# Performance work log

Measured on AMD Instinct MI355X. Metric: run time of the kernel, lower is better.

Reference implementation:

```python
import jax, jax.numpy as jnp
import numpy as np

N = 100000
NEG_SLOPE = 0.2
EPS = 1e-16


def _gatconv(h_in, src, dst, W, a_src, a_dst, b):
    # h_in: [N, Fin]; src/dst: [E_tot] (self-loops included); W: [Fin, Fout]
    h = h_in @ W                                  # [N, Fout]
    alpha_s = h @ a_src                           # [N]
    alpha_d = h @ a_dst                           # [N]
    e = alpha_s[src] + alpha_d[dst]               # [E_tot]
    e = jnp.where(e > 0, e, NEG_SLOPE * e)        # leaky_relu
    m = jax.ops.segment_max(e, dst, num_segments=N)
    e = jnp.exp(e - m[dst])
    s = jax.ops.segment_sum(e, dst, num_segments=N)
    alpha = e / (s[dst] + EPS)                    # segment softmax over in-edges of each dst
    out = jax.ops.segment_sum(alpha[:, None] * h[src], dst, num_segments=N)
    return out + b


def setup_inputs() -> dict:
    key = jax.random.key(0)
    ks = jax.random.split(key, 10)
    Fin, Fh, Fo = 64, 64, 40
    E = 1600000
    x = jax.random.normal(ks[0], (N, Fin), dtype=jnp.float32)
    edge_index = jax.random.randint(ks[1], (2, E), 0, N, dtype=jnp.int64)
    g = 1.0 / np.sqrt(Fin)
    W1 = jax.random.uniform(ks[2], (Fin, Fh), jnp.float32, -g, g)
    a_src1 = jax.random.uniform(ks[3], (Fh,), jnp.float32, -g, g)
    a_dst1 = jax.random.uniform(ks[4], (Fh,), jnp.float32, -g, g)
    b1 = jnp.zeros((Fh,), jnp.float32)
    g2 = 1.0 / np.sqrt(Fh)
    W2 = jax.random.uniform(ks[5], (Fh, Fo), jnp.float32, -g2, g2)
    a_src2 = jax.random.uniform(ks[6], (Fo,), jnp.float32, -g2, g2)
    a_dst2 = jax.random.uniform(ks[7], (Fo,), jnp.float32, -g2, g2)
    b2 = jnp.zeros((Fo,), jnp.float32)
    return {"x": x, "edge_index": edge_index, "W1": W1, "a_src1": a_src1,
            "a_dst1": a_dst1, "b1": b1, "W2": W2, "a_src2": a_src2,
            "a_dst2": a_dst2, "b2": b2}


def reference(x, edge_index, W1, a_src1, a_dst1, b1, W2, a_src2, a_dst2, b2):
    # add self loops (PyG GATConv default)
    loops = jnp.arange(N, dtype=edge_index.dtype)
    src = jnp.concatenate([edge_index[0], loops])
    dst = jnp.concatenate([edge_index[1], loops])
    h = _gatconv(x, src, dst, W1, a_src1, a_dst1, b1)
    h = jax.nn.relu(h)  # dropout p=0 / eval -> no-op
    h = _gatconv(h, src, dst, W2, a_src2, a_dst2, b2)
    return jax.nn.log_softmax(h, axis=-1)
```

## Files before the change

kernel.cpp:

```cpp
#include <hip/hip_runtime.h>
#include <math.h>

#ifndef NEG_SLOPE
#define NEG_SLOPE 0.2f
#endif

#define BUCK_BITS 9
#define BUCK_SIZE 512
#define BUCK_CAP  12288
#define PA_ILP    8
#define SMAX      0x1FFFF

typedef __attribute__((ext_vector_type(8))) short bhalf8;
typedef __attribute__((ext_vector_type(4))) float f32x4;

__device__ __forceinline__ void get_edge(const void* ei, int is64, int e, int E,
                                         int& s, int& d) {
    if (e >= E) { s = e - E; d = s; return; }
    if (is64) {
        const long long* p = (const long long*)ei;
        s = (int)p[e];
        d = (int)p[(long long)E + e];
    } else {
        const int* p = (const int*)ei;
        s = p[e];
        d = p[E + e];
    }
}

__device__ __forceinline__ unsigned f2bf1(float x) {
    unsigned u = __float_as_uint(x);
    return (u + 0x7fffu + ((u >> 16) & 1u)) >> 16;
}

__global__ __launch_bounds__(256) void bin_gemm1(
    const void* __restrict__ ei, int E, int Etot, int binB, int gemmB, int period,
    int* __restrict__ fill, unsigned* __restrict__ pairs,
    const float* __restrict__ x, const float* __restrict__ W1,
    const float* __restrict__ avs, const float* __restrict__ avd,
    unsigned short* __restrict__ Hb, float* __restrict__ asn,
    float* __restrict__ adn, int N) {
    __shared__ __align__(16) char smem[16896];
    const int t = threadIdx.x;
    const int bi = blockIdx.x;
    const bool isBin = (bi % period) == 0;

    if (isBin) {
        const int bb = bi / period;
        int* cnt   = (int*)smem;
        int* goff  = cnt + 256;
        int* sflag = goff + 256;
        if (t < 64) {
            const int* p = (const int*)ei;
            int bad = 0;
            for (int j = 0; j < 4; ++j) bad |= (p[2 * (t * 4 + j) + 1] != 0);
            unsigned long long m = __ballot(bad);
            if (t == 0) *sflag = (m == 0ull) ? 1 : 0;
        }
        cnt[t] = 0;
        __syncthreads();
        const int is64 = *sflag;
        const int base = bb * (256 * PA_ILP) + t;
        int s[PA_ILP], d[PA_ILP], r[PA_ILP];
        bool ok[PA_ILP];
#pragma unroll
        for (int u = 0; u < PA_ILP; ++u) {
            int e = base + u * 256;
            ok[u] = (e < Etot);
            s[u] = d[u] = 0;
            if (ok[u]) get_edge(ei, is64, e, E, s[u], d[u]);
        }
#pragma unroll
        for (int u = 0; u < PA_ILP; ++u)
            if (ok[u]) r[u] = atomicAdd(&cnt[d[u] >> BUCK_BITS], 1);
        __syncthreads();
        if (cnt[t] > 0) goff[t] = atomicAdd(&fill[t], cnt[t]);
        __syncthreads();
#pragma unroll
        for (int u = 0; u < PA_ILP; ++u) {
            if (ok[u]) {
                int b = d[u] >> BUCK_BITS;
                int idx = goff[b] + r[u];
                if (idx < BUCK_CAP)
                    pairs[(size_t)b * BUCK_CAP + idx] =
                        (unsigned)s[u] | ((unsigned)(d[u] & (BUCK_SIZE - 1)) << 17);
            }
        }
    } else {
        const int gi = bi - bi / period - 1;
        if (gi >= gemmB) return;
        constexpr int K = 64, F = 64, TPR = 4, R = 64, C = 16;
        float* sW  = (float*)smem;
        float* sas = sW + K * F;
        float* sad = sas + F;

        for (int i = t; i < K * F / 4; i += 256)
            ((float4*)sW)[i] = ((const float4*)W1)[i];
        if (t < F) { sas[t] = avs[t]; sad[t] = avd[t]; }
        __syncthreads();

        const int base = gi * R;
        const int r  = t / TPR;
        const int f0 = (t % TPR) * C;
        const int row = base + r;
        float acc[C];
#pragma unroll
        for (int j = 0; j < C; ++j) acc[j] = 0.f;
        if (row < N) {
            const float4* xr = (const float4*)(x + (size_t)row * K);
#pragma unroll
            for (int c4 = 0; c4 < 16; ++c4) {
                float4 a = xr[c4];
                const float* w0 = &sW[(c4 * 4 + 0) * F + f0];
                const float* w1 = &sW[(c4 * 4 + 1) * F + f0];
                const float* w2 = &sW[(c4 * 4 + 2) * F + f0];
                const float* w3 = &sW[(c4 * 4 + 3) * F + f0];
#pragma unroll
                for (int j = 0; j < C; ++j)
                    acc[j] += a.x * w0[j] + a.y * w1[j] + a.z * w2[j] + a.w * w3[j];
            }
        }
        float ps = 0.f, pd = 0.f;
#pragma unroll
        for (int j = 0; j < C; ++j) { ps += acc[j] * sas[f0 + j]; pd += acc[j] * sad[f0 + j]; }
#pragma unroll
        for (int off = 1; off < TPR; off <<= 1) {
            ps += __shfl_xor(ps, off);
            pd += __shfl_xor(pd, off);
        }
        if (row < N) {
            if ((t % TPR) == 0) { asn[row] = ps; adn[row] = pd; }
            unsigned* hp = (unsigned*)(Hb + (size_t)row * F + f0);
#pragma unroll
            for (int j = 0; j < C / 2; ++j)
                hp[j] = f2bf1(acc[2 * j]) | (f2bf1(acc[2 * j + 1]) << 16);
        }
    }
}

__global__ __launch_bounds__(256) void bucket_csr(
    const unsigned* __restrict__ pairs, const int* __restrict__ fill,
    int* __restrict__ row_ptr, int* __restrict__ csr_src, int N, int nbuck) {
    __shared__ int cnt[BUCK_SIZE];
    __shared__ int offs[BUCK_SIZE];
    __shared__ int sbase[256];
    __shared__ int stot;
    const int t = threadIdx.x;
    if (t < 64) {
        int v[4];
        int loc = 0;
#pragma unroll
        for (int i = 0; i < 4; ++i) {
            int idx = t * 4 + i;
            v[i] = (idx < nbuck) ? fill[idx] : 0;
            loc += v[i];
        }
        int x = loc;
        for (int off = 1; off < 64; off <<= 1) {
            int y = __shfl_up(x, off);
            if (t >= off) x += y;
        }
        int run = x - loc;
#pragma unroll
        for (int i = 0; i < 4; ++i) {
            int idx = t * 4 + i;
            if (idx < 256) sbase[idx] = run;
            run += v[i];
        }
        if (t == 63) stot = x;
    }
    cnt[t] = 0; cnt[t + 256] = 0;
    __syncthreads();

    const int b = blockIdx.x;
    const int gb = sbase[b];
    int m = fill[b];
    if (m > BUCK_CAP) m = BUCK_CAP;
    if (b == 0 && t == 0) row_ptr[N] = stot;
    const unsigned* bp = pairs + (size_t)b * BUCK_CAP;

    int i = t;
    for (; i + 768 < m; i += 1024) {
        unsigned p0 = bp[i], p1 = bp[i + 256], p2 = bp[i + 512], p3 = bp[i + 768];
        atomicAdd(&cnt[p0 >> 17], 1);
        atomicAdd(&cnt[p1 >> 17], 1);
        atomicAdd(&cnt[p2 >> 17], 1);
        atomicAdd(&cnt[p3 >> 17], 1);
    }
    for (; i < m; i += 256) atomicAdd(&cnt[bp[i] >> 17], 1);
    __syncthreads();

    if (t < 64) {
        int v[8];
        int loc = 0;
#pragma unroll
        for (int j = 0; j < 8; ++j) { v[j] = cnt[t * 8 + j]; loc += v[j]; }
        int x = loc;
        for (int off = 1; off < 64; off <<= 1) {
            int y = __shfl_up(x, off);
            if (t >= off) x += y;
        }
        int run = x - loc;
#pragma unroll
        for (int j = 0; j < 8; ++j) { offs[t * 8 + j] = gb + run; run += v[j]; }
    }
    __syncthreads();

    const int base_d = b << BUCK_BITS;
    for (int k = t; k < BUCK_SIZE; k += 256) {
        int d = base_d + k;
        if (d < N) row_ptr[d] = offs[k];
    }
    __syncthreads();

    i = t;
    for (; i + 768 < m; i += 1024) {
        unsigned p0 = bp[i], p1 = bp[i + 256], p2 = bp[i + 512], p3 = bp[i + 768];
        csr_src[atomicAdd(&offs[p0 >> 17], 1)] = p0 & SMAX;
        csr_src[atomicAdd(&offs[p1 >> 17], 1)] = p1 & SMAX;
        csr_src[atomicAdd(&offs[p2 >> 17], 1)] = p2 & SMAX;
        csr_src[atomicAdd(&offs[p3 >> 17], 1)] = p3 & SMAX;
    }
    for (; i < m; i += 256) {
        unsigned p = bp[i];
        csr_src[atomicAdd(&offs[p >> 17], 1)] = p & SMAX;
    }
}

__device__ __forceinline__ void bf16x8_fma(uint4 hv, float w, float* acc) {
    const unsigned* u = (const unsigned*)&hv;
#pragma unroll
    for (int i = 0; i < 4; ++i) {
        float lo = __uint_as_float(u[i] << 16);
        float hi = __uint_as_float(u[i] & 0xffff0000u);
        acc[2 * i]     += w * lo;
        acc[2 * i + 1] += w * hi;
    }
}

__global__ __launch_bounds__(256) void agg1_gemm2(
    const int* __restrict__ row_ptr, const int* __restrict__ csr_src,
    const float* __restrict__ asn1, const float* __restrict__ adn1,
    const unsigned short* __restrict__ Hb, const float* __restrict__ b1,
    const float* __restrict__ W2, const float* __restrict__ a_s2,
    const float* __restrict__ a_d2, unsigned short* __restrict__ Hb2,
    float* __restrict__ asn2, float* __restrict__ adn2, int N) {
    __shared__ __align__(16) unsigned short rb16[16][72];
    __shared__ float sa2[48], sd2[48], sb1[64];
    __shared__ float sps3[3][16], spd3[3][16];
    const int t = threadIdx.x;
    if (t < 48) {
        sa2[t] = (t < 40) ? a_s2[t] : 0.f;
        sd2[t] = (t < 40) ? a_d2[t] : 0.f;
    }
    if (t >= 64 && t < 128) sb1[t - 64] = b1[t - 64];

    const int lane = t & 63;
    const int wv   = t >> 6;
    const int tile = (wv < 3) ? wv : 0;

    bhalf8 bfr[2];
    {
        const int col = tile * 16 + (lane & 15);
        const int kb  = (lane >> 4) * 8;
        const bool cv = col < 40;
#pragma unroll
        for (int ks = 0; ks < 2; ++ks) {
            bhalf8 bb;
#pragma unroll
            for (int j = 0; j < 8; ++j) {
                float v = cv ? W2[(size_t)(kb + 32 * ks + j) * 40 + col] : 0.f;
                bb[j] = (short)f2bf1(v);
            }
            bfr[ks] = bb;
        }
    }
    __syncthreads();

    const int sub     = lane & 15;
    const int half    = sub >> 3;
    const int q       = sub & 7;
    const int grpbase = lane & 48;
    const int slot    = t >> 4;
    const int node    = blockIdx.x * 16 + slot;
    const bool valid  = node < N;
    const int nd      = valid ? node : N - 1;

    const int r0 = row_ptr[nd], r1 = row_ptr[nd + 1];
    const int deg = r1 - r0;
    const float add = adn1[nd];

    float acc[8];
#pragma unroll
    for (int i = 0; i < 8; ++i) acc[i] = 0.f;

    int   sA = 0, sB = 0;
    float wA = 0.f, wB = 0.f;
    {
        const bool vA = sub < deg;
        const bool vB = 16 + sub < deg;
        if (vA) sA = csr_src[r0 + sub];
        if (vB) sB = csr_src[r0 + 16 + sub];
        float aA = vA ? asn1[sA] : 0.f;
        float aB = vB ? asn1[sB] : 0.f;
        if (vA) { float v = aA + add; v = v > 0.f ? v : NEG_SLOPE * v; wA = __expf(v); }
        if (vB) { float v = aB + add; v = v > 0.f ? v : NEG_SLOPE * v; wB = __expf(v); }
    }
    float Ssum = wA + wB;

    {
        const int cnt = deg < 16 ? deg : 16;
        int se[8]; float we[8]; uint4 hv[8];
#pragma unroll
        for (int k = 0; k < 8; ++k) {
            int e = 2 * k + half;
            int sl = grpbase | (e & 15);
            se[k] = __shfl(sA, sl);
            float wk = __shfl(wA, sl);
            we[k] = (e < cnt) ? wk : 0.f;
        }
#pragma unroll
        for (int k = 0; k < 4; ++k)
            hv[k] = *(const uint4*)(Hb + (((unsigned)se[k] << 6) | (unsigned)(q << 3)));
        if (cnt > 8) {
#pragma unroll
            for (int k = 4; k < 8; ++k)
                hv[k] = *(const uint4*)(Hb + (((unsigned)se[k] << 6) | (unsigned)(q << 3)));
        }
#pragma unroll
        for (int k = 0; k < 4; ++k) bf16x8_fma(hv[k], we[k], acc);
        if (cnt > 8) {
#pragma unroll
            for (int k = 4; k < 8; ++k) bf16x8_fma(hv[k], we[k], acc);
        }
    }
    if (deg > 16) {
        const int cnt = (deg - 16) < 16 ? (deg - 16) : 16;
        int se[8]; float we[8]; uint4 hv[8];
#pragma unroll
        for (int k = 0; k < 8; ++k) {
            int e = 2 * k + half;
            int sl = grpbase | (e & 15);
            se[k] = __shfl(sB, sl);
            float wk = __shfl(wB, sl);
            we[k] = (e < cnt) ? wk : 0.f;
        }
#pragma unroll
        for (int k = 0; k < 4; ++k)
            hv[k] = *(const uint4*)(Hb + (((unsigned)se[k] << 6) | (unsigned)(q << 3)));
        if (cnt > 8) {
#pragma unroll
            for (int k = 4; k < 8; ++k)
                hv[k] = *(const uint4*)(Hb + (((unsigned)se[k] << 6) | (unsigned)(q << 3)));
        }
#pragma unroll
        for (int k = 0; k < 4; ++k) bf16x8_fma(hv[k], we[k], acc);
        if (cnt > 8) {
#pragma unroll
            for (int k = 4; k < 8; ++k) bf16x8_fma(hv[k], we[k], acc);
        }
    }
    for (int base = r0 + 32; base < r1; base += 16) {
        int cnt = r1 - base;
        if (cnt > 16) cnt = 16;
        int s = 0;
        float w = 0.f;
        if (sub < cnt) {
            s = csr_src[base + sub];
            float v = asn1[s] + add;
            v = v > 0.f ? v : NEG_SLOPE * v;
            w = __expf(v);
        }
        Ssum += w;
        for (int j = 0; j < cnt; j += 8) {
            int se[4]; float we[4]; uint4 hv[4];
#pragma unroll
            for (int k = 0; k < 4; ++k) {
                int e = j + 2 * k + half;
                int src_lane = grpbase | (e & 15);
                se[k] = __shfl(s, src_lane);
                float wk = __shfl(w, src_lane);
                we[k] = (e < cnt) ? wk : 0.f;
            }
#pragma unroll
            for (int k = 0; k < 4; ++k)
                hv[k] = *(const uint4*)(Hb + (((unsigned)se[k] << 6) | (unsigned)(q << 3)));
#pragma unroll
            for (int k = 0; k < 4; ++k) bf16x8_fma(hv[k], we[k], acc);
        }
    }
#pragma unroll
    for (int i = 0; i < 8; ++i) acc[i] += __shfl_xor(acc[i], 8);
#pragma unroll
    for (int off = 1; off < 16; off <<= 1) Ssum += __shfl_xor(Ssum, off);
    const float inv = 1.f / (Ssum + 1e-16f);

    if (half == 0) {
        unsigned pk[4];
#pragma unroll
        for (int i = 0; i < 4; ++i) {
            float v0 = fmaxf(acc[2 * i]     * inv + sb1[q * 8 + 2 * i],     0.f);
            float v1 = fmaxf(acc[2 * i + 1] * inv + sb1[q * 8 + 2 * i + 1], 0.f);
            pk[i] = f2bf1(v0) | (f2bf1(v1) << 16);
        }
        *(uint4*)&rb16[slot][q * 8] = make_uint4(pk[0], pk[1], pk[2], pk[3]);
    }
    __syncthreads();

    if (wv < 3) {
        f32x4 dacc = {0.f, 0.f, 0.f, 0.f};
#pragma unroll
        for (int ks = 0; ks < 2; ++ks) {
            bhalf8 afr = *(const bhalf8*)&rb16[lane & 15][(lane >> 4) * 8 + 32 * ks];
            dacc = __builtin_amdgcn_mfma_f32_16x16x32_bf16(afr, bfr[ks], dacc, 0, 0, 0);
        }
        const int f   = tile * 16 + (lane & 15);
        const float saf = sa2[f];
        const float sdf = sd2[f];
        float psl = 0.f, pdl = 0.f;
#pragma unroll
        for (int i = 0; i < 4; ++i) {
            psl = dacc[i] * saf;
            pdl = dacc[i] * sdf;
#pragma unroll
            for (int off = 1; off < 16; off <<= 1) {
                psl += __shfl_xor(psl, off);
                pdl += __shfl_xor(pdl, off);
            }
            const int m  = (lane >> 4) * 4 + i;
            if ((lane & 15) == 0) { sps3[tile][m] = psl; spd3[tile][m] = pdl; }
            const int nn = blockIdx.x * 16 + m;
            if (f < 40 && nn < N)
                Hb2[(size_t)nn * 40 + f] = (unsigned short)f2bf1(dacc[i]);
        }
    }
    __syncthreads();
    if (t < 16) {
        const int nn = blockIdx.x * 16 + t;
        if (nn < N) {
            asn2[nn] = sps3[0][t] + sps3[1][t] + sps3[2][t];
            adn2[nn] = spd3[0][t] + spd3[1][t] + spd3[2][t];
        }
    }
}

__global__ __launch_bounds__(256) void agg2_lsm(
    const int* __restrict__ row_ptr, const int* __restrict__ csr_src,
    const float* __restrict__ asn, const float* __restrict__ adn,
    const unsigned short* __restrict__ Hb, const float* __restrict__ bias,
    float* __restrict__ out, int N) {
    const int lane    = threadIdx.x & 63;
    const int sub     = lane & 15;
    const int esl     = sub / 5;
    const int q5      = sub - esl * 5;
    const bool act    = sub < 15;
    const int qc      = act ? q5 : 0;
    const float qmask = act ? 1.f : 0.f;
    const int grpbase = lane & 48;
    const int node    = blockIdx.x * 16 + (threadIdx.x >> 4);
    const bool valid  = node < N;
    const int nd      = valid ? node : N - 1;

    const int r0 = row_ptr[nd], r1 = row_ptr[nd + 1];
    const int deg = r1 - r0;
    const float add = adn[nd];

    float acc[8];
#pragma unroll
    for (int i = 0; i < 8; ++i) acc[i] = 0.f;

    int   sA = 0, sB = 0;
    float wA = 0.f, wB = 0.f;
    {
        const bool vA = sub < deg;
        const bool vB = 16 + sub < deg;
        if (vA) sA = csr_src[r0 + sub];
        if (vB) sB = csr_src[r0 + 16 + sub];
        float aA = vA ? asn[sA] : 0.f;
        float aB = vB ? asn[sB] : 0.f;
        if (vA) { float v = aA + add; v = v > 0.f ? v : NEG_SLOPE * v; wA = __expf(v); }
        if (vB) { float v = aB + add; v = v > 0.f ? v : NEG_SLOPE * v; wB = __expf(v); }
    }
    float Ssum = wA + wB;

    {
        const int cnt = deg < 16 ? deg : 16;
        int se[6]; float we[6]; uint4 hv[6];
#pragma unroll
        for (int kk = 0; kk < 6; ++kk) {
            int e  = 3 * kk + esl;
            int el = (e < 16) ? e : 15;
            se[kk] = __shfl(sA, grpbase | el);
            float wk = __shfl(wA, grpbase | el) * qmask;
            we[kk] = (e < cnt) ? wk : 0.f;
        }
#pragma unroll
        for (int kk = 0; kk < 4; ++kk)
            hv[kk] = *(const uint4*)(Hb + ((unsigned)se[kk] * 40u + (unsigned)(qc << 3)));
        if (cnt > 12) {
#pragma unroll
            for (int kk = 4; kk < 6; ++kk)
                hv[kk] = *(const uint4*)(Hb + ((unsigned)se[kk] * 40u + (unsigned)(qc << 3)));
        }
#pragma unroll
        for (int kk = 0; kk < 4; ++kk) bf16x8_fma(hv[kk], we[kk], acc);
        if (cnt > 12) {
#pragma unroll
            for (int kk = 4; kk < 6; ++kk) bf16x8_fma(hv[kk], we[kk], acc);
        }
    }
    if (deg > 16) {
        const int cnt = (deg - 16) < 16 ? (deg - 16) : 16;
        int se[6]; float we[6]; uint4 hv[6];
#pragma unroll
        for (int kk = 0; kk < 6; ++kk) {
            int e  = 3 * kk + esl;
            int el = (e < 16) ? e : 15;
            se[kk] = __shfl(sB, grpbase | el);
            float wk = __shfl(wB, grpbase | el) * qmask;
            we[kk] = (e < cnt) ? wk : 0.f;
        }
#pragma unroll
        for (int kk = 0; kk < 4; ++kk)
            hv[kk] = *(const uint4*)(Hb + ((unsigned)se[kk] * 40u + (unsigned)(qc << 3)));
        if (cnt > 12) {
#pragma unroll
            for (int kk = 4; kk < 6; ++kk)
                hv[kk] = *(const uint4*)(Hb + ((unsigned)se[kk] * 40u + (unsigned)(qc << 3)));
        }
#pragma unroll
        for (int kk = 0; kk < 4; ++kk) bf16x8_fma(hv[kk], we[kk], acc);
        if (cnt > 12) {
#pragma unroll
            for (int kk = 4; kk < 6; ++kk) bf16x8_fma(hv[kk], we[kk], acc);
        }
    }
    for (int base = r0 + 32; base < r1; base += 16) {
        int cnt = r1 - base;
        if (cnt > 16) cnt = 16;
        int s = 0;
        float w = 0.f;
        if (sub < cnt) {
            s = csr_src[base + sub];
            float v = asn[s] + add;
            v = v > 0.f ? v : NEG_SLOPE * v;
            w = __expf(v);
        }
        Ssum += w;
        for (int j = 0; j < cnt; j += 12) {
            int se[4]; float we[4]; uint4 hv[4];
#pragma unroll
            for (int k = 0; k < 4; ++k) {
                int e  = j + 3 * k + esl;
                int el = (e < 16) ? e : 15;
                se[k] = __shfl(s, grpbase | el);
                float wk = __shfl(w, grpbase | el) * qmask;
                we[k] = (e < cnt) ? wk : 0.f;
            }
#pragma unroll
            for (int k = 0; k < 4; ++k)
                hv[k] = *(const uint4*)(Hb + ((unsigned)se[k] * 40u + (unsigned)(qc << 3)));
#pragma unroll
            for (int k = 0; k < 4; ++k) bf16x8_fma(hv[k], we[k], acc);
        }
    }
#pragma unroll
    for (int i = 0; i < 8; ++i) {
        float a1 = __shfl(acc[i], grpbase + q5 + 5);
        float a2 = __shfl(acc[i], grpbase + q5 + 10);
        acc[i] += a1 + a2;
    }
#pragma unroll
    for (int off = 1; off < 16; off <<= 1) Ssum += __shfl_xor(Ssum, off);
    const float inv = 1.f / (Ssum + 1e-16f);
    const bool owner = act && (esl == 0);

    float val[8];
#pragma unroll
    for (int i = 0; i < 8; ++i) val[i] = acc[i] * inv + bias[qc * 8 + i];
    float mx = -3.0e38f;
    if (owner) {
#pragma unroll
        for (int i = 0; i < 8; ++i) mx = fmaxf(mx, val[i]);
    }
#pragma unroll
    for (int off = 1; off <= 8; off <<= 1) mx = fmaxf(mx, __shfl_xor(mx, off));
    float sm = 0.f;
    if (owner) {
#pragma unroll
        for (int i = 0; i < 8; ++i) sm += __expf(val[i] - mx);
    }
#pragma unroll
    for (int off = 1; off <= 8; off <<= 1) sm += __shfl_xor(sm, off);
    float ls = logf(sm) + mx;
    if (valid && owner) {
        float* op = out + (size_t)node * 40 + q5 * 8;
        ((float4*)op)[0] = make_float4(val[0] - ls, val[1] - ls, val[2] - ls, val[3] - ls);
        ((float4*)op)[1] = make_float4(val[4] - ls, val[5] - ls, val[6] - ls, val[7] - ls);
    }
}

extern "C" void kernel_launch(void* const* d_in, const int* in_sizes, int n_in,
                              void* d_out, int out_size, void* d_ws, size_t ws_size,
                              hipStream_t stream) {
    const float* x   = (const float*)d_in[0];
    const void*  ei  = d_in[1];
    const float* W1  = (const float*)d_in[2];
    const float* as1 = (const float*)d_in[3];
    const float* ad1 = (const float*)d_in[4];
    const float* b1  = (const float*)d_in[5];
    const float* W2  = (const float*)d_in[6];
    const float* as2 = (const float*)d_in[7];
    const float* ad2 = (const float*)d_in[8];
    const float* b2  = (const float*)d_in[9];
    float* out = (float*)d_out;

    const int N     = in_sizes[0] / 64;
    const int E     = in_sizes[1] / 2;
    const int Etot  = E + N;
    const int nbuck = (N + BUCK_SIZE - 1) >> BUCK_BITS;

    float* ws = (float*)d_ws;
    unsigned short* hb  = (unsigned short*)ws;  ws += (size_t)N * 32;
    unsigned short* hb2 = (unsigned short*)ws;  ws += (size_t)N * 20;
    float* asn1 = ws;              ws += N;
    float* adn1 = ws;              ws += N;
    float* asn2 = ws;              ws += N;
    float* adn2 = ws;              ws += N;
    int* row_ptr = (int*)ws;       ws += N + 1;
    int* csr_src = (int*)ws;       ws += Etot;
    int* fill   = (int*)ws;        ws += 256;
    unsigned* pairs = (unsigned*)ws;  ws += (size_t)256 * BUCK_CAP;

    const int binB   = (Etot + 256 * PA_ILP - 1) / (256 * PA_ILP);
    const int gemmB  = (N + 63) / 64;
    const int period = gemmB / binB + 2;
    const int grid1  = binB * period;
    const int AGG_B  = (N + 15) / 16;

    hipMemsetAsync(fill, 0, 256 * sizeof(int), stream);
    bin_gemm1<<<grid1, 256, 0, stream>>>(
        ei, E, Etot, binB, gemmB, period, fill, pairs,
        x, W1, as1, ad1, hb, asn1, adn1, N);
    bucket_csr<<<nbuck, 256, 0, stream>>>(pairs, fill, row_ptr, csr_src, N, nbuck);
    agg1_gemm2<<<AGG_B, 256, 0, stream>>>(
        row_ptr, csr_src, asn1, adn1, hb, b1, W2, as2, ad2, hb2, asn2, adn2, N);
    agg2_lsm<<<AGG_B, 256, 0, stream>>>(
        row_ptr, csr_src, asn2, adn2, hb2, b2, out, N);
}
```

Before: 220.9 us.

## Compute layer-1 GEMM with split-bf16 MFMA instead of scalar FMA

Replaces the scalar-FMA x@W1 path in the fused bin/GEMM kernel with MFMA 16x16x32 bf16 instructions. Inputs and weights are split into high and low bf16 parts and combined with three MFMAs to stay close to fp32 accuracy. W1 is read straight from global memory per lane instead of being staged in LDS, which cuts the kernel's shared memory from about 16.5KB to 4KB and may raise occupancy. The risks are uncoalesced 2-byte Hb stores, scattered W reads, and a small accuracy loss from the split-bf16 scheme.

```diff
diff --git a/kernel.cpp b/kernel.cpp
--- a/kernel.cpp
+++ b/kernel.cpp
@@ -40,7 +40,7 @@
     const float* __restrict__ avs, const float* __restrict__ avd,
     unsigned short* __restrict__ Hb, float* __restrict__ asn,
     float* __restrict__ adn, int N) {
-    __shared__ __align__(16) char smem[16896];
+    __shared__ __align__(16) char smem[4096];
     const int t = threadIdx.x;
     const int bi = blockIdx.x;
     const bool isBin = (bi % period) == 0;
@@ -89,51 +89,89 @@
     } else {
         const int gi = bi - bi / period - 1;
         if (gi >= gemmB) return;
-        constexpr int K = 64, F = 64, TPR = 4, R = 64, C = 16;
-        float* sW  = (float*)smem;
-        float* sas = sW + K * F;
-        float* sad = sas + F;
-
-        for (int i = t; i < K * F / 4; i += 256)
-            ((float4*)sW)[i] = ((const float4*)W1)[i];
-        if (t < F) { sas[t] = avs[t]; sad[t] = avd[t]; }
-        __syncthreads();
-
-        const int base = gi * R;
-        const int r  = t / TPR;
-        const int f0 = (t % TPR) * C;
-        const int row = base + r;
-        float acc[C];
-#pragma unroll
-        for (int j = 0; j < C; ++j) acc[j] = 0.f;
-        if (row < N) {
-            const float4* xr = (const float4*)(x + (size_t)row * K);
-#pragma unroll
-            for (int c4 = 0; c4 < 16; ++c4) {
-                float4 a = xr[c4];
-                const float* w0 = &sW[(c4 * 4 + 0) * F + f0];
-                const float* w1 = &sW[(c4 * 4 + 1) * F + f0];
-                const float* w2 = &sW[(c4 * 4 + 2) * F + f0];
-                const float* w3 = &sW[(c4 * 4 + 3) * F + f0];
-#pragma unroll
-                for (int j = 0; j < C; ++j)
-                    acc[j] += a.x * w0[j] + a.y * w1[j] + a.z * w2[j] + a.w * w3[j];
-            }
-        }
-        float ps = 0.f, pd = 0.f;
-#pragma unroll
-        for (int j = 0; j < C; ++j) { ps += acc[j] * sas[f0 + j]; pd += acc[j] * sad[f0 + j]; }
-#pragma unroll
-        for (int off = 1; off < TPR; off <<= 1) {
-            ps += __shfl_xor(ps, off);
-            pd += __shfl_xor(pd, off);
-        }
-        if (row < N) {
-            if ((t % TPR) == 0) { asn[row] = ps; adn[row] = pd; }
-            unsigned* hp = (unsigned*)(Hb + (size_t)row * F + f0);
-#pragma unroll
-            for (int j = 0; j < C / 2; ++j)
-                hp[j] = f2bf1(acc[2 * j]) | (f2bf1(acc[2 * j + 1]) << 16);
+        const int lane = t & 63;
+        const int w    = t >> 6;
+        const int rloc = lane & 15;
+        const int kg   = lane >> 4;
+        const int base = gi * 64;
+        const int row  = base + w * 16 + rloc;
+        const int rowc = (row < N) ? row : (N - 1);
+
+        bhalf8 xh[2], xl[2];
+        {
+            const float* xr = x + (size_t)rowc * 64;
+#pragma unroll
+            for (int ks = 0; ks < 2; ++ks) {
+                const int k0 = kg * 8 + ks * 32;
+                float4 a0 = *(const float4*)(xr + k0);
+                float4 a1 = *(const float4*)(xr + k0 + 4);
+                float av[8] = {a0.x, a0.y, a0.z, a0.w, a1.x, a1.y, a1.z, a1.w};
+                bhalf8 h8, l8;
+#pragma unroll
+                for (int j = 0; j < 8; ++j) {
+                    unsigned hb_ = f2bf1(av[j]);
+                    float hf = __uint_as_float(hb_ << 16);
+                    h8[j] = (short)hb_;
+                    l8[j] = (short)f2bf1(av[j] - hf);
+                }
+                xh[ks] = h8;
+                xl[ks] = l8;
+            }
+        }
+
+        f32x4 dacc[4];
+#pragma unroll
+        for (int ct = 0; ct < 4; ++ct) dacc[ct] = (f32x4){0.f, 0.f, 0.f, 0.f};
+
+#pragma unroll
+        for (int ct = 0; ct < 4; ++ct) {
+            const int col = ct * 16 + rloc;
+#pragma unroll
+            for (int ks = 0; ks < 2; ++ks) {
+                const int k0 = kg * 8 + ks * 32;
+                bhalf8 bh, bl;
+#pragma unroll
+                for (int j = 0; j < 8; ++j) {
+                    float wv_ = W1[(size_t)(k0 + j) * 64 + col];
+                    unsigned hb_ = f2bf1(wv_);
+                    float hf = __uint_as_float(hb_ << 16);
+                    bh[j] = (short)hb_;
+                    bl[j] = (short)f2bf1(wv_ - hf);
+                }
+                dacc[ct] = __builtin_amdgcn_mfma_f32_16x16x32_bf16(xh[ks], bh, dacc[ct], 0, 0, 0);
+                dacc[ct] = __builtin_amdgcn_mfma_f32_16x16x32_bf16(xl[ks], bh, dacc[ct], 0, 0, 0);
+                dacc[ct] = __builtin_amdgcn_mfma_f32_16x16x32_bf16(xh[ks], bl, dacc[ct], 0, 0, 0);
+            }
+        }
+
+        float sa[4], sd[4];
+#pragma unroll
+        for (int ct = 0; ct < 4; ++ct) {
+            sa[ct] = avs[ct * 16 + rloc];
+            sd[ct] = avd[ct * 16 + rloc];
+        }
+#pragma unroll
+        for (int i = 0; i < 4; ++i) {
+            float ps = 0.f, pd = 0.f;
+#pragma unroll
+            for (int ct = 0; ct < 4; ++ct) {
+                float h = dacc[ct][i];
+                ps += h * sa[ct];
+                pd += h * sd[ct];
+            }
+#pragma unroll
+            for (int off = 1; off < 16; off <<= 1) {
+                ps += __shfl_xor(ps, off);
+                pd += __shfl_xor(pd, off);
+            }
+            const int gr = base + w * 16 + kg * 4 + i;
+            if (gr < N) {
+                if (rloc == 0) { asn[gr] = ps; adn[gr] = pd; }
+#pragma unroll
+                for (int ct = 0; ct < 4; ++ct)
+                    Hb[(size_t)gr * 64 + ct * 16 + rloc] =
+                        (unsigned short)f2bf1(dacc[ct][i]);
+            }
         }
     }
 }
```

Measured after the change: 220.1 us. About the same (-0.3%).
